# Kernel optimization log

Hardware: AMD Instinct MI355X
Metric: run time of the kernel (lower is better)

The kernel has to match this reference:

```python
import jax, jax.numpy as jnp
import numpy as np

EMBED_DIM = 1024
NUM_HEADS = 16
HEAD_DIM = EMBED_DIM // NUM_HEADS
T, B = 2048, 2


def setup_inputs() -> dict:
    key = jax.random.key(0)
    ks = jax.random.split(key, 12)
    s = 1.0 / np.sqrt(EMBED_DIM)
    x = jax.random.normal(ks[0], (T, B, EMBED_DIM), dtype=jnp.float32)
    time_decay = jax.random.uniform(ks[1], (T, B, 1), dtype=jnp.float32)
    # causal mask: masked_fill where mask == 0
    attn_mask = jnp.tril(jnp.ones((T, T), dtype=jnp.int32))
    Wq = jax.random.uniform(ks[2], (EMBED_DIM, EMBED_DIM), jnp.float32, -s, s)
    bq = jax.random.uniform(ks[3], (EMBED_DIM,), jnp.float32, -s, s)
    Wk = jax.random.uniform(ks[4], (EMBED_DIM, EMBED_DIM), jnp.float32, -s, s)
    bk = jax.random.uniform(ks[5], (EMBED_DIM,), jnp.float32, -s, s)
    Wv = jax.random.uniform(ks[6], (EMBED_DIM, EMBED_DIM), jnp.float32, -s, s)
    bv = jax.random.uniform(ks[7], (EMBED_DIM,), jnp.float32, -s, s)
    Wo = jax.random.uniform(ks[8], (EMBED_DIM, EMBED_DIM), jnp.float32, -s, s)
    bo = jax.random.uniform(ks[9], (EMBED_DIM,), jnp.float32, -s, s)
    return {"x": x, "time_decay": time_decay, "attn_mask": attn_mask,
            "Wq": Wq, "bq": bq, "Wk": Wk, "bk": bk,
            "Wv": Wv, "bv": bv, "Wo": Wo, "bo": bo}


def reference(x, time_decay, attn_mask, Wq, bq, Wk, bk, Wv, bv, Wo, bo):
    t, b, e = x.shape
    h, d = NUM_HEADS, HEAD_DIM
    # linear (torch: y = x @ W.T + b), then split heads -> (B, H, T, D)
    def proj(W, bias):
        y = jnp.einsum('tbe,fe->tbf', x, W) + bias
        return y.reshape(t, b, h, d).transpose(1, 2, 0, 3)
    Q, K, V = proj(Wq, bq), proj(Wk, bk), proj(Wv, bv)
    scores = jnp.einsum('bhqd,bhkd->bhqk', Q, K) / np.sqrt(d).astype(jnp.float32)
    scores = jnp.where(attn_mask == 0, jnp.float32(-1e9), scores)
    attn = jax.nn.softmax(scores, axis=-1)
    out = jnp.einsum('bhqk,bhkd->bhqd', attn, V)      # (B,H,T,D)
    out = out.transpose(2, 0, 1, 3).reshape(t, b, e)   # (T,B,E)
    out = jnp.einsum('tbe,fe->tbf', out, Wo) + bo
    return out * time_decay
```

## Files before the change

kernel.cpp:

```cpp
#include <hip/hip_runtime.h>


typedef unsigned short u16;
typedef __attribute__((ext_vector_type(8))) short bf16x8_t;
typedef __attribute__((ext_vector_type(4))) float fx4_t;

#define T_SEQ 2048
#define BATCH 2
#define EMB   1024
#define NH    16
#define HD    64
#define MROWS (T_SEQ * BATCH)

#define EXP2F(x) __builtin_amdgcn_exp2f(x)

__device__ __forceinline__ float bf2f(u16 u) {
  union { unsigned int i; float f; } v;
  v.i = ((unsigned int)u) << 16;
  return v.f;
}
__device__ __forceinline__ u16 f2bf(float f) {
  union { float f; unsigned int i; } v;
  v.f = f;
  unsigned int x = v.i;
  unsigned int r = (x + 0x7fffu + ((x >> 16) & 1u)) >> 16;
  return (u16)r;
}

__device__ __forceinline__ void glds16(const void* g, void* l) {
  __builtin_amdgcn_global_load_lds(
      (const __attribute__((address_space(1))) unsigned int*)g,
      (__attribute__((address_space(3))) unsigned int*)l, 16, 0, 0);
}

__global__ void cvt_all(const float* __restrict__ x,
                        const float* __restrict__ wq, const float* __restrict__ wk,
                        const float* __restrict__ wv, const float* __restrict__ wo,
                        u16* __restrict__ xb,
                        u16* __restrict__ wqb, u16* __restrict__ wkb,
                        u16* __restrict__ wvb, u16* __restrict__ wob) {
  int i = blockIdx.x * blockDim.x + threadIdx.x;
  const float* src; u16* dst; int off;
  if (i < 1048576)      { src = x;  dst = xb;  off = i; }
  else if (i < 1310720) { src = wq; dst = wqb; off = i - 1048576; }
  else if (i < 1572864) { src = wk; dst = wkb; off = i - 1310720; }
  else if (i < 1835008) { src = wv; dst = wvb; off = i - 1572864; }
  else                  { src = wo; dst = wob; off = i - 1835008; }
  float4 v = ((const float4*)src)[off];
  ushort4 o;
  o.x = f2bf(v.x); o.y = f2bf(v.y); o.z = f2bf(v.z); o.w = f2bf(v.w);
  ((ushort4*)dst)[off] = o;
}

__global__ __launch_bounds__(256, 2) void gemm_qkv(
    const u16* __restrict__ xb,
    const u16* __restrict__ wq, const u16* __restrict__ wk, const u16* __restrict__ wv,
    const float* __restrict__ bq, const float* __restrict__ bk, const float* __restrict__ bv,
    u16* __restrict__ Qh, u16* __restrict__ Kh, u16* __restrict__ VTg) {
  __shared__ short As[128 * 64];
  __shared__ short Bs[128 * 64];

  const int z = blockIdx.z;
  const u16* W = (z == 0) ? wq : (z == 1) ? wk : wv;
  const float* bias = (z == 0) ? bq : (z == 1) ? bk : bv;

  const int tid = threadIdx.x;
  const int bm = blockIdx.x, bn = blockIdx.y;
  const int lane = tid & 63, w = tid >> 6;
  const int wm = w >> 1, wn = w & 1;
  const int lr = lane & 15, quad = lane >> 4;
  const int r0 = lane >> 3, c8 = (lane & 7) * 8;

  fx4_t acc[4][4];
#pragma unroll
  for (int i = 0; i < 4; i++)
#pragma unroll
    for (int j = 0; j < 4; j++) acc[i][j] = (fx4_t){0.f, 0.f, 0.f, 0.f};

  for (int k0 = 0; k0 < EMB; k0 += 64) {
#pragma unroll
    for (int i = 0; i < 4; i++) {
      const int rr = w * 32 + i * 8;
      glds16(xb + (size_t)(bm * 128 + rr + r0) * EMB + k0 + c8, &As[rr * 64]);
      glds16(W  + (size_t)(bn * 128 + rr + r0) * EMB + k0 + c8, &Bs[rr * 64]);
    }
    __syncthreads();
#pragma unroll
    for (int ks = 0; ks < 2; ++ks) {
      bf16x8_t a[4], b[4];
      const int goff = (ks * 4 + quad) * 8;
#pragma unroll
      for (int i = 0; i < 4; i++) a[i] = *(const bf16x8_t*)&As[(wm * 64 + i * 16 + lr) * 64 + goff];
#pragma unroll
      for (int j = 0; j < 4; j++) b[j] = *(const bf16x8_t*)&Bs[(wn * 64 + j * 16 + lr) * 64 + goff];
#pragma unroll
      for (int i = 0; i < 4; i++)
#pragma unroll
        for (int j = 0; j < 4; j++)
          acc[i][j] = __builtin_amdgcn_mfma_f32_16x16x32_bf16(a[i], b[j], acc[i][j], 0, 0, 0);
    }
    __syncthreads();
  }

#pragma unroll
  for (int i = 0; i < 4; i++) {
#pragma unroll
    for (int j = 0; j < 4; j++) {
      const int n = bn * 128 + wn * 64 + j * 16 + lr;
      const float bsv = bias[n];
      const int h = n >> 6, d = n & 63;
#pragma unroll
      for (int r = 0; r < 4; r++) {
        const int m = bm * 128 + wm * 64 + i * 16 + quad * 4 + r;
        const int t = m >> 1, bb = m & 1;
        float v = acc[i][j][r] + bsv;
        if (z == 2) {
          VTg[((size_t)(bb * NH + h) * HD + d) * T_SEQ + t] = f2bf(v);
        } else {
          u16* dst = (z == 0) ? Qh : Kh;
          dst[((size_t)(bb * NH + h) * T_SEQ + t) * HD + d] = f2bf(v);
        }
      }
    }
  }
}

__global__ __launch_bounds__(256, 2) void gemm_out(
    const u16* __restrict__ Ob, const u16* __restrict__ wo,
    const float* __restrict__ bo, const float* __restrict__ td,
    float* __restrict__ out) {
  __shared__ short As[64 * 64];
  __shared__ short Bs[128 * 64];

  const int tid = threadIdx.x;
  const int bm = blockIdx.x, bn = blockIdx.y;
  const int lane = tid & 63, w = tid >> 6;
  const int wm = w >> 1, wn = w & 1;
  const int lr = lane & 15, quad = lane >> 4;
  const int r0 = lane >> 3, c8 = (lane & 7) * 8;

  fx4_t acc[2][4];
#pragma unroll
  for (int i = 0; i < 2; i++)
#pragma unroll
    for (int j = 0; j < 4; j++) acc[i][j] = (fx4_t){0.f, 0.f, 0.f, 0.f};

  for (int k0 = 0; k0 < EMB; k0 += 64) {
#pragma unroll
    for (int i = 0; i < 2; i++) {
      const int rr = w * 16 + i * 8;
      glds16(Ob + (size_t)(bm * 64 + rr + r0) * EMB + k0 + c8, &As[rr * 64]);
    }
#pragma unroll
    for (int i = 0; i < 4; i++) {
      const int rr = w * 32 + i * 8;
      glds16(wo + (size_t)(bn * 128 + rr + r0) * EMB + k0 + c8, &Bs[rr * 64]);
    }
    __syncthreads();
#pragma unroll
    for (int ks = 0; ks < 2; ++ks) {
      bf16x8_t a[2], b[4];
      const int goff = (ks * 4 + quad) * 8;
#pragma unroll
      for (int i = 0; i < 2; i++) a[i] = *(const bf16x8_t*)&As[(wm * 32 + i * 16 + lr) * 64 + goff];
#pragma unroll
      for (int j = 0; j < 4; j++) b[j] = *(const bf16x8_t*)&Bs[(wn * 64 + j * 16 + lr) * 64 + goff];
#pragma unroll
      for (int i = 0; i < 2; i++)
#pragma unroll
        for (int j = 0; j < 4; j++)
          acc[i][j] = __builtin_amdgcn_mfma_f32_16x16x32_bf16(a[i], b[j], acc[i][j], 0, 0, 0);
    }
    __syncthreads();
  }

#pragma unroll
  for (int i = 0; i < 2; i++) {
#pragma unroll
    for (int j = 0; j < 4; j++) {
      const int n = bn * 128 + wn * 64 + j * 16 + lr;
      const float bsv = bo[n];
#pragma unroll
      for (int r = 0; r < 4; r++) {
        const int m = bm * 64 + wm * 32 + i * 16 + quad * 4 + r;
        out[(size_t)m * EMB + n] = (acc[i][j][r] + bsv) * td[m];
      }
    }
  }
}

__global__ __launch_bounds__(256, 3) void attn_mfma3(
    const u16* __restrict__ Qh, const u16* __restrict__ Kh, const u16* __restrict__ VTg,
    u16* __restrict__ Ob) {
  __shared__ short Kd[2][64 * 64];
  __shared__ short Vd[2][64 * 64];
  __shared__ short Ps[4][16 * 72];

  const int blk = blockIdx.x;
  const int bh = blk & 31;
  const int j = blk >> 5;
  const int qt = (j & 1) ? (31 - (j >> 1)) : (j >> 1);
  const int qb = qt * 64;

  const int tid = threadIdx.x;
  const int w = tid >> 6, lane = tid & 63;
  const int lr = lane & 15, quad = lane >> 4;
  const int r0 = lane >> 3, c8 = (lane & 7) * 8;

  const u16* Qb = Qh + (size_t)bh * T_SEQ * HD;
  const u16* Kb = Kh + (size_t)bh * T_SEQ * HD;
  const u16* VTb = VTg + (size_t)bh * HD * T_SEQ;

  const float QSCALE = 0.18033688f;
  bf16x8_t qf[2];
#pragma unroll
  for (int ks = 0; ks < 2; ks++) {
    bf16x8_t v = *(const bf16x8_t*)(Qb + (size_t)(qb + w * 16 + lr) * HD + ks * 32 + quad * 8);
    bf16x8_t o;
#pragma unroll
    for (int e = 0; e < 8; e++) o[e] = (short)f2bf(bf2f((u16)v[e]) * QSCALE);
    qf[ks] = o;
  }

  fx4_t acc_o[4];
#pragma unroll
  for (int dn = 0; dn < 4; dn++) acc_o[dn] = (fx4_t){0.f, 0.f, 0.f, 0.f};
  float m_i = -1e30f, l_i = 0.f;

#define STAGE(kt_, buf_)                                                          \
  {                                                                               \
    const int k0_ = (kt_) * 64;                                                   \
    _Pragma("unroll")                                                             \
    for (int i = 0; i < 2; i++) {                                                 \
      const int rr = w * 16 + i * 8;                                              \
      glds16(Kb + (size_t)(k0_ + rr + r0) * HD + c8, &Kd[buf_][rr * 64]);         \
      glds16(VTb + (size_t)(rr + r0) * T_SEQ + k0_ + c8, &Vd[buf_][rr * 64]);     \
    }                                                                             \
  }

  const int nkt = qt + 1;
  STAGE(0, 0);
  __syncthreads();

  for (int kt = 0; kt < nkt; kt++) {
    const int buf = kt & 1;
    if (kt + 1 < nkt) STAGE(kt + 1, buf ^ 1);

    fx4_t st[4];
#pragma unroll
    for (int nt = 0; nt < 4; nt++) st[nt] = (fx4_t){0.f, 0.f, 0.f, 0.f};
#pragma unroll
    for (int ks = 0; ks < 2; ks++) {
#pragma unroll
      for (int nt = 0; nt < 4; nt++) {
        bf16x8_t kf = *(const bf16x8_t*)&Kd[buf][(nt * 16 + lr) * 64 + ks * 32 + quad * 8];
        st[nt] = __builtin_amdgcn_mfma_f32_16x16x32_bf16(kf, qf[ks], st[nt], 0, 0, 0);
      }
    }

    if (kt == qt) {
#pragma unroll
      for (int nt = 0; nt < 4; nt++)
#pragma unroll
        for (int r = 0; r < 4; r++)
          if (nt * 16 + quad * 4 + r > w * 16 + lr) st[nt][r] = -1e30f;
    }

    float rmax = -1e30f;
#pragma unroll
    for (int nt = 0; nt < 4; nt++)
#pragma unroll
      for (int r = 0; r < 4; r++) rmax = fmaxf(rmax, st[nt][r]);
    rmax = fmaxf(rmax, __shfl_xor(rmax, 16));
    rmax = fmaxf(rmax, __shfl_xor(rmax, 32));
    const float mn = fmaxf(m_i, rmax);
    const float alpha = EXP2F(m_i - mn);
    m_i = mn;
    float rsum = 0.f;
#pragma unroll
    for (int nt = 0; nt < 4; nt++) {
#pragma unroll
      for (int r = 0; r < 4; r++) {
        float e = EXP2F(st[nt][r] - mn);
        st[nt][r] = e;
        rsum += e;
      }
    }
    rsum += __shfl_xor(rsum, 16);
    rsum += __shfl_xor(rsum, 32);
    l_i = l_i * alpha + rsum;

    short* Pw = Ps[w];
#pragma unroll
    for (int nt = 0; nt < 4; nt++) {
      short4 pv;
      pv.x = (short)f2bf(st[nt][0]);
      pv.y = (short)f2bf(st[nt][1]);
      pv.z = (short)f2bf(st[nt][2]);
      pv.w = (short)f2bf(st[nt][3]);
      *(short4*)&Pw[lr * 72 + nt * 16 + quad * 4] = pv;
    }

#pragma unroll
    for (int r = 0; r < 4; r++) {
      const float a_r = __shfl(alpha, quad * 4 + r);
#pragma unroll
      for (int dn = 0; dn < 4; dn++) acc_o[dn][r] *= a_r;
    }

#pragma unroll
    for (int ks = 0; ks < 2; ks++) {
      bf16x8_t pf = *(const bf16x8_t*)&Pw[lr * 72 + ks * 32 + quad * 8];
#pragma unroll
      for (int dn = 0; dn < 4; dn++) {
        bf16x8_t vf = *(const bf16x8_t*)&Vd[buf][(dn * 16 + lr) * 64 + ks * 32 + quad * 8];
        acc_o[dn] = __builtin_amdgcn_mfma_f32_16x16x32_bf16(pf, vf, acc_o[dn], 0, 0, 0);
      }
    }

    __syncthreads();
  }
#undef STAGE

  const float inv = 1.0f / l_i;
  const int b = bh >> 4, h = bh & 15;
#pragma unroll
  for (int r = 0; r < 4; r++) {
    const float inv_r = __shfl(inv, quad * 4 + r);
    const int t = qb + w * 16 + quad * 4 + r;
#pragma unroll
    for (int dn = 0; dn < 4; dn++) {
      const int d = dn * 16 + lr;
      Ob[(size_t)(t * BATCH + b) * EMB + h * HD + d] = f2bf(acc_o[dn][r] * inv_r);
    }
  }
}

extern "C" void kernel_launch(void* const* d_in, const int* in_sizes, int n_in,
                              void* d_out, int out_size, void* d_ws, size_t ws_size,
                              hipStream_t stream) {
  const float* x  = (const float*)d_in[0];
  const float* td = (const float*)d_in[1];
  const float* Wq = (const float*)d_in[3];
  const float* bq = (const float*)d_in[4];
  const float* Wk = (const float*)d_in[5];
  const float* bk = (const float*)d_in[6];
  const float* Wv = (const float*)d_in[7];
  const float* bv = (const float*)d_in[8];
  const float* Wo = (const float*)d_in[9];
  const float* bo = (const float*)d_in[10];
  float* out = (float*)d_out;

  char* ws = (char*)d_ws;
  u16* xb  = (u16*)(ws + 0);
  u16* wqb = (u16*)(ws + ((size_t)8  << 20));
  u16* wkb = (u16*)(ws + ((size_t)10 << 20));
  u16* wvb = (u16*)(ws + ((size_t)12 << 20));
  u16* wob = (u16*)(ws + ((size_t)14 << 20));
  u16* Qh  = (u16*)(ws + ((size_t)16 << 20));
  u16* Kh  = (u16*)(ws + ((size_t)24 << 20));
  u16* VTg = (u16*)(ws + ((size_t)32 << 20));
  u16* Ob  = xb;

  cvt_all<<<8192, 256, 0, stream>>>(x, Wq, Wk, Wv, Wo, xb, wqb, wkb, wvb, wob);

  gemm_qkv<<<dim3(MROWS / 128, EMB / 128, 3), 256, 0, stream>>>(
      xb, wqb, wkb, wvb, bq, bk, bv, Qh, Kh, VTg);

  attn_mfma3<<<1024, 256, 0, stream>>>(Qh, Kh, VTg, Ob);

  gemm_out<<<dim3(MROWS / 64, EMB / 128), 256, 0, stream>>>(Ob, wob, bo, td, out);
}
```

Before: 229.8 us.

## XOR-swizzle LDS tiles, store Q/K row-major, transpose V via swapped MFMA

Applies an XOR swizzle to the LDS column offsets in both GEMMs and the attention kernel, which should cut bank conflicts on the 128-byte-stride bf16x8 reads. Q and K are now written in plain token-major (T,B,E) layout, and attention reads them with a 2*EMB row stride instead of a head-major scatter. For V, the GEMM reorders its input rows so each block's rows are batch-grouped, then swaps the MFMA operands so the accumulator's lane dimension runs along tokens. This should make the transposed V^T stores more contiguous. The cost is extra index math, and the strided Q/K reads in attention may coalesce less well.

```diff
diff --git a/kernel.cpp b/kernel.cpp
--- a/kernel.cpp
+++ b/kernel.cpp
@@ -32,6 +32,7 @@
       (const __attribute__((address_space(1))) unsigned int*)g,
       (__attribute__((address_space(3))) unsigned int*)l, 16, 0, 0);
 }
+
 
 __global__ void cvt_all(const float* __restrict__ x,
                         const float* __restrict__ wq, const float* __restrict__ wk,
@@ -56,7 +57,7 @@
     const u16* __restrict__ xb,
     const u16* __restrict__ wq, const u16* __restrict__ wk, const u16* __restrict__ wv,
     const float* __restrict__ bq, const float* __restrict__ bk, const float* __restrict__ bv,
-    u16* __restrict__ Qh, u16* __restrict__ Kh, u16* __restrict__ VTg) {
+    u16* __restrict__ Qm, u16* __restrict__ Km, u16* __restrict__ VTg) {
   __shared__ short As[128 * 64];
   __shared__ short Bs[128 * 64];
 
@@ -69,7 +70,9 @@
   const int lane = tid & 63, w = tid >> 6;
   const int wm = w >> 1, wn = w & 1;
   const int lr = lane & 15, quad = lane >> 4;
-  const int r0 = lane >> 3, c8 = (lane & 7) * 8;
+  const int r0 = lane >> 3;
+  const int c8s = ((lane & 7) ^ r0) * 8;
+  const int sw = (lr & 7);
 
   fx4_t acc[4][4];
 #pragma unroll
@@ -81,44 +84,65 @@
 #pragma unroll
     for (int i = 0; i < 4; i++) {
       const int rr = w * 32 + i * 8;
-      glds16(xb + (size_t)(bm * 128 + rr + r0) * EMB + k0 + c8, &As[rr * 64]);
-      glds16(W  + (size_t)(bn * 128 + rr + r0) * EMB + k0 + c8, &Bs[rr * 64]);
+      const int ml = bm * 128 + rr + r0;
+      const int grow = (z == 2) ? (((ml & 2047) << 1) | (ml >> 11)) : ml;
+      glds16(xb + (size_t)grow * EMB + k0 + c8s, &As[rr * 64]);
+      glds16(W + (size_t)(bn * 128 + rr + r0) * EMB + k0 + c8s, &Bs[rr * 64]);
     }
     __syncthreads();
 #pragma unroll
     for (int ks = 0; ks < 2; ++ks) {
       bf16x8_t a[4], b[4];
-      const int goff = (ks * 4 + quad) * 8;
-#pragma unroll
-      for (int i = 0; i < 4; i++) a[i] = *(const bf16x8_t*)&As[(wm * 64 + i * 16 + lr) * 64 + goff];
-#pragma unroll
-      for (int j = 0; j < 4; j++) b[j] = *(const bf16x8_t*)&Bs[(wn * 64 + j * 16 + lr) * 64 + goff];
 #pragma unroll
       for (int i = 0; i < 4; i++)
-#pragma unroll
-        for (int j = 0; j < 4; j++)
-          acc[i][j] = __builtin_amdgcn_mfma_f32_16x16x32_bf16(a[i], b[j], acc[i][j], 0, 0, 0);
+        a[i] = *(const bf16x8_t*)&As[(wm * 64 + i * 16 + lr) * 64 + (((ks * 4 + quad) ^ sw) * 8)];
+#pragma unroll
+      for (int j = 0; j < 4; j++)
+        b[j] = *(const bf16x8_t*)&Bs[(wn * 64 + j * 16 + lr) * 64 + (((ks * 4 + quad) ^ sw) * 8)];
+      if (z == 2) {
+#pragma unroll
+        for (int i = 0; i < 4; i++)
+#pragma unroll
+          for (int j = 0; j < 4; j++)
+            acc[i][j] = __builtin_amdgcn_mfma_f32_16x16x32_bf16(b[j], a[i], acc[i][j], 0, 0, 0);
+      } else {
+#pragma unroll
+        for (int i = 0; i < 4; i++)
+#pragma unroll
+          for (int j = 0; j < 4; j++)
+            acc[i][j] = __builtin_amdgcn_mfma_f32_16x16x32_bf16(a[i], b[j], acc[i][j], 0, 0, 0);
+      }
     }
     __syncthreads();
   }
 
-#pragma unroll
-  for (int i = 0; i < 4; i++) {
-#pragma unroll
-    for (int j = 0; j < 4; j++) {
-      const int n = bn * 128 + wn * 64 + j * 16 + lr;
-      const float bsv = bias[n];
-      const int h = n >> 6, d = n & 63;
-#pragma unroll
-      for (int r = 0; r < 4; r++) {
-        const int m = bm * 128 + wm * 64 + i * 16 + quad * 4 + r;
-        const int t = m >> 1, bb = m & 1;
-        float v = acc[i][j][r] + bsv;
-        if (z == 2) {
-          VTg[((size_t)(bb * NH + h) * HD + d) * T_SEQ + t] = f2bf(v);
-        } else {
-          u16* dst = (z == 0) ? Qh : Kh;
-          dst[((size_t)(bb * NH + h) * T_SEQ + t) * HD + d] = f2bf(v);
+  if (z == 2) {
+#pragma unroll
+    for (int i = 0; i < 4; i++) {
+#pragma unroll
+      for (int j = 0; j < 4; j++) {
+#pragma unroll
+        for (int r = 0; r < 4; r++) {
+          const int n = bn * 128 + wn * 64 + j * 16 + quad * 4 + r;
+          const int ml = bm * 128 + wm * 64 + i * 16 + lr;
+          const int t = ml & 2047, bb = ml >> 11;
+          const int h = n >> 6, d = n & 63;
+          VTg[((size_t)(bb * NH + h) * HD + d) * T_SEQ + t] = f2bf(acc[i][j][r] + bias[n]);
+        }
+      }
+    }
+  } else {
+    u16* dst = (z == 0) ? Qm : Km;
+#pragma unroll
+    for (int i = 0; i < 4; i++) {
+#pragma unroll
+      for (int j = 0; j < 4; j++) {
+        const int n = bn * 128 + wn * 64 + j * 16 + lr;
+        const float bsv = bias[n];
+#pragma unroll
+        for (int r = 0; r < 4; r++) {
+          const int m = bm * 128 + wm * 64 + i * 16 + quad * 4 + r;
+          dst[(size_t)m * EMB + n] = f2bf(acc[i][j][r] + bsv);
         }
       }
     }
@@ -137,7 +161,9 @@
   const int lane = tid & 63, w = tid >> 6;
   const int wm = w >> 1, wn = w & 1;
   const int lr = lane & 15, quad = lane >> 4;
-  const int r0 = lane >> 3, c8 = (lane & 7) * 8;
+  const int r0 = lane >> 3;
+  const int c8s = ((lane & 7) ^ r0) * 8;
+  const int sw = (lr & 7);
 
   fx4_t acc[2][4];
 #pragma unroll
@@ -149,22 +175,23 @@
 #pragma unroll
     for (int i = 0; i < 2; i++) {
       const int rr = w * 16 + i * 8;
-      glds16(Ob + (size_t)(bm * 64 + rr + r0) * EMB + k0 + c8, &As[rr * 64]);
+      glds16(Ob + (size_t)(bm * 64 + rr + r0) * EMB + k0 + c8s, &As[rr * 64]);
     }
 #pragma unroll
     for (int i = 0; i < 4; i++) {
       const int rr = w * 32 + i * 8;
-      glds16(wo + (size_t)(bn * 128 + rr + r0) * EMB + k0 + c8, &Bs[rr * 64]);
+      glds16(wo + (size_t)(bn * 128 + rr + r0) * EMB + k0 + c8s, &Bs[rr * 64]);
     }
     __syncthreads();
 #pragma unroll
     for (int ks = 0; ks < 2; ++ks) {
       bf16x8_t a[2], b[4];
-      const int goff = (ks * 4 + quad) * 8;
-#pragma unroll
-      for (int i = 0; i < 2; i++) a[i] = *(const bf16x8_t*)&As[(wm * 32 + i * 16 + lr) * 64 + goff];
-#pragma unroll
-      for (int j = 0; j < 4; j++) b[j] = *(const bf16x8_t*)&Bs[(wn * 64 + j * 16 + lr) * 64 + goff];
+#pragma unroll
+      for (int i = 0; i < 2; i++)
+        a[i] = *(const bf16x8_t*)&As[(wm * 32 + i * 16 + lr) * 64 + (((ks * 4 + quad) ^ sw) * 8)];
+#pragma unroll
+      for (int j = 0; j < 4; j++)
+        b[j] = *(const bf16x8_t*)&Bs[(wn * 64 + j * 16 + lr) * 64 + (((ks * 4 + quad) ^ sw) * 8)];
 #pragma unroll
       for (int i = 0; i < 2; i++)
 #pragma unroll
@@ -189,8 +216,8 @@
   }
 }
 
-__global__ __launch_bounds__(256, 3) void attn_mfma3(
-    const u16* __restrict__ Qh, const u16* __restrict__ Kh, const u16* __restrict__ VTg,
+__global__ __launch_bounds__(256, 3) void attn_mfma6(
+    const u16* __restrict__ Qm, const u16* __restrict__ Km, const u16* __restrict__ VTg,
     u16* __restrict__ Ob) {
   __shared__ short Kd[2][64 * 64];
   __shared__ short Vd[2][64 * 64];
@@ -201,21 +228,24 @@
   const int j = blk >> 5;
   const int qt = (j & 1) ? (31 - (j >> 1)) : (j >> 1);
   const int qb = qt * 64;
+  const int b = bh >> 4, h = bh & 15;
 
   const int tid = threadIdx.x;
   const int w = tid >> 6, lane = tid & 63;
   const int lr = lane & 15, quad = lane >> 4;
-  const int r0 = lane >> 3, c8 = (lane & 7) * 8;
-
-  const u16* Qb = Qh + (size_t)bh * T_SEQ * HD;
-  const u16* Kb = Kh + (size_t)bh * T_SEQ * HD;
+  const int r0 = lane >> 3;
+  const int c8s = ((lane & 7) ^ r0) * 8;
+  const int sw = (lr & 7);
+
+  const u16* Qbase = Qm + (size_t)b * EMB + (size_t)h * HD;
+  const u16* Kbase = Km + (size_t)b * EMB + (size_t)h * HD;
   const u16* VTb = VTg + (size_t)bh * HD * T_SEQ;
 
   const float QSCALE = 0.18033688f;
   bf16x8_t qf[2];
 #pragma unroll
   for (int ks = 0; ks < 2; ks++) {
-    bf16x8_t v = *(const bf16x8_t*)(Qb + (size_t)(qb + w * 16 + lr) * HD + ks * 32 + quad * 8);
+    bf16x8_t v = *(const bf16x8_t*)(Qbase + (size_t)(qb + w * 16 + lr) * 2 * EMB + ks * 32 + quad * 8);
     bf16x8_t o;
 #pragma unroll
     for (int e = 0; e < 8; e++) o[e] = (short)f2bf(bf2f((u16)v[e]) * QSCALE);
@@ -227,15 +257,15 @@
   for (int dn = 0; dn < 4; dn++) acc_o[dn] = (fx4_t){0.f, 0.f, 0.f, 0.f};
   float m_i = -1e30f, l_i = 0.f;
 
-#define STAGE(kt_, buf_)                                                          \
-  {                                                                               \
-    const int k0_ = (kt_) * 64;                                                   \
-    _Pragma("unroll")                                                             \
-    for (int i = 0; i < 2; i++) {                                                 \
-      const int rr = w * 16 + i * 8;                                              \
-      glds16(Kb + (size_t)(k0_ + rr + r0) * HD + c8, &Kd[buf_][rr * 64]);         \
-      glds16(VTb + (size_t)(rr + r0) * T_SEQ + k0_ + c8, &Vd[buf_][rr * 64]);     \
-    }                                                                             \
+#define STAGE(kt_, buf_)                                                            \
+  {                                                                                 \
+    const int k0_ = (kt_) * 64;                                                     \
+    _Pragma("unroll")                                                               \
+    for (int i = 0; i < 2; i++) {                                                   \
+      const int rr = w * 16 + i * 8;                                                \
+      glds16(Kbase + (size_t)(k0_ + rr + r0) * 2 * EMB + c8s, &Kd[buf_][rr * 64]);  \
+      glds16(VTb + (size_t)(rr + r0) * T_SEQ + k0_ + c8s, &Vd[buf_][rr * 64]);      \
+    }                                                                               \
   }
 
   const int nkt = qt + 1;
@@ -253,7 +283,7 @@
     for (int ks = 0; ks < 2; ks++) {
 #pragma unroll
       for (int nt = 0; nt < 4; nt++) {
-        bf16x8_t kf = *(const bf16x8_t*)&Kd[buf][(nt * 16 + lr) * 64 + ks * 32 + quad * 8];
+        bf16x8_t kf = *(const bf16x8_t*)&Kd[buf][(nt * 16 + lr) * 64 + (((ks * 4 + quad) ^ sw) * 8)];
         st[nt] = __builtin_amdgcn_mfma_f32_16x16x32_bf16(kf, qf[ks], st[nt], 0, 0, 0);
       }
     }
@@ -313,7 +343,7 @@
       bf16x8_t pf = *(const bf16x8_t*)&Pw[lr * 72 + ks * 32 + quad * 8];
 #pragma unroll
       for (int dn = 0; dn < 4; dn++) {
-        bf16x8_t vf = *(const bf16x8_t*)&Vd[buf][(dn * 16 + lr) * 64 + ks * 32 + quad * 8];
+        bf16x8_t vf = *(const bf16x8_t*)&Vd[buf][(dn * 16 + lr) * 64 + (((ks * 4 + quad) ^ sw) * 8)];
         acc_o[dn] = __builtin_amdgcn_mfma_f32_16x16x32_bf16(pf, vf, acc_o[dn], 0, 0, 0);
       }
     }
@@ -323,7 +353,6 @@
 #undef STAGE
 
   const float inv = 1.0f / l_i;
-  const int b = bh >> 4, h = bh & 15;
 #pragma unroll
   for (int r = 0; r < 4; r++) {
     const float inv_r = __shfl(inv, quad * 4 + r);
@@ -357,17 +386,17 @@
   u16* wkb = (u16*)(ws + ((size_t)10 << 20));
   u16* wvb = (u16*)(ws + ((size_t)12 << 20));
   u16* wob = (u16*)(ws + ((size_t)14 << 20));
-  u16* Qh  = (u16*)(ws + ((size_t)16 << 20));
-  u16* Kh  = (u16*)(ws + ((size_t)24 << 20));
+  u16* Qm  = (u16*)(ws + ((size_t)16 << 20));
+  u16* Km  = (u16*)(ws + ((size_t)24 << 20));
   u16* VTg = (u16*)(ws + ((size_t)32 << 20));
   u16* Ob  = xb;
 
   cvt_all<<<8192, 256, 0, stream>>>(x, Wq, Wk, Wv, Wo, xb, wqb, wkb, wvb, wob);
 
   gemm_qkv<<<dim3(MROWS / 128, EMB / 128, 3), 256, 0, stream>>>(
-      xb, wqb, wkb, wvb, bq, bk, bv, Qh, Kh, VTg);
-
-  attn_mfma3<<<1024, 256, 0, stream>>>(Qh, Kh, VTg, Ob);
+      xb, wqb, wkb, wvb, bq, bk, bv, Qm, Km, VTg);
+
+  attn_mfma6<<<1024, 256, 0, stream>>>(Qm, Km, VTg, Ob);
 
   gemm_out<<<dim3(MROWS / 64, EMB / 128), 256, 0, stream>>>(Ob, wob, bo, td, out);
 }
```

Measured after the change: 204.6 us. -10.9%, faster.
